# Kernel optimization log

Measured on AMD Instinct MI355X. Metric: run time of the kernel, lower is better.

## Reference

```python
import jax, jax.numpy as jnp
import numpy as np

D_MODEL = 2048
N_HEADS = 16
HEAD_DIM = D_MODEL // N_HEADS
LN_EPS = 1e-6  # flax.linen.LayerNorm default
NEG_INF = float('-inf')


def _layernorm_scale_only(x, scale):
    # flax LayerNorm with use_bias=False: normalize over last axis, scale only
    mean = jnp.mean(x, axis=-1, keepdims=True)
    var = jnp.var(x, axis=-1, keepdims=True)
    return (x - mean) * jax.lax.rsqrt(var + LN_EPS) * scale


def setup_inputs() -> dict:
    key = jax.random.key(0)
    ks = jax.random.split(key, 4)
    B, S = 2, 2048
    x = jax.random.normal(ks[0], (B, S, D_MODEL), dtype=jnp.float32)
    Wqkv = jax.random.normal(ks[1], (D_MODEL, 3 * D_MODEL), dtype=jnp.float32) * 0.02
    q_ln_scale = jnp.ones((D_MODEL,), dtype=jnp.float32)
    k_ln_scale = jnp.ones((D_MODEL,), dtype=jnp.float32)
    out_W = jax.random.normal(ks[2], (D_MODEL, D_MODEL), dtype=jnp.float32) * 0.02
    return {"x": x, "Wqkv": Wqkv, "q_ln_scale": q_ln_scale,
            "k_ln_scale": k_ln_scale, "out_W": out_W}


def reference(x, Wqkv, q_ln_scale, k_ln_scale, out_W):
    B, S, _ = x.shape
    qkv = jnp.einsum('bsd,de->bse', x, Wqkv)  # [B,S,3*D] (no bias)
    q, k, v = jnp.split(qkv, 3, axis=-1)
    # QK LayerNorm (attn_qk_ln=True, no bias)
    q = _layernorm_scale_only(q, q_ln_scale)
    k = _layernorm_scale_only(k, k_ln_scale)
    # split heads: [B,S,H,Dh]
    q = q.reshape(B, S, N_HEADS, HEAD_DIM)
    k = k.reshape(B, S, N_HEADS, HEAD_DIM)
    v = v.reshape(B, S, N_HEADS, HEAD_DIM)
    # scaled scores [B,H,S,S]
    scores = jnp.einsum('bshd,bthd->bhst', q / jnp.sqrt(jnp.float32(HEAD_DIM)), k)
    # causal mask: triu(ones, k=1) marks strictly-future positions -> -inf
    causal = jnp.triu(jnp.ones((S, S), dtype=bool), 1)
    scores = jnp.where(causal, NEG_INF, scores)
    # kv-cache mask: arange(S) < S - past_position - S = 0 -> all False (no-op
    # with past_position=0 and no layer_past), faithfully omitted.
    attn = jax.nn.softmax(scores, axis=-1)
    ctx = jnp.einsum('bhst,bthd->bshd', attn, v)  # [B,S,H,Dh]
    out = jnp.einsum('bsd,de->bse', ctx.reshape(B, S, D_MODEL), out_W)
    return out
```

## Files before the change

### kernel.cpp

```cpp
#include <hip/hip_runtime.h>


typedef float f32x4 __attribute__((ext_vector_type(4)));
typedef short s16x8 __attribute__((ext_vector_type(8)));
typedef short s16x4 __attribute__((ext_vector_type(4)));

static __device__ __forceinline__ unsigned short f2bf(float f) {
  unsigned u = __builtin_bit_cast(unsigned, f);
  unsigned r = u + 0x7fffu + ((u >> 16) & 1u);
  return (unsigned short)(r >> 16);
}
static __device__ __forceinline__ float bf2f(unsigned short s) {
  unsigned u = ((unsigned)s) << 16;
  return __builtin_bit_cast(float, u);
}

static __device__ __forceinline__ void gload_lds16(const unsigned short* g, unsigned short* l) {
  __builtin_amdgcn_global_load_lds((const __attribute__((address_space(1))) void*)g,
                                   (__attribute__((address_space(3))) void*)l, 16, 0, 0);
}

__global__ __launch_bounds__(256) void k_cvt4(const float4* __restrict__ in,
                                              s16x4* __restrict__ out, int n) {
  int i = blockIdx.x * 256 + threadIdx.x;
  if (i >= n) return;
  float4 v = in[i];
  s16x4 o = { (short)f2bf(v.x), (short)f2bf(v.y), (short)f2bf(v.z), (short)f2bf(v.w) };
  out[i] = o;
}

__global__ __launch_bounds__(256) void k_twT(const float* __restrict__ in,
                                             unsigned short* __restrict__ out,
                                             int K, int N) {
  __shared__ float tile[32][33];
  const int n0 = blockIdx.x * 32, k0 = blockIdx.y * 32;
  const int tx = threadIdx.x & 31, ty = threadIdx.x >> 5;
#pragma unroll
  for (int rr = 0; rr < 4; ++rr) {
    int kr = ty + rr * 8;
    tile[kr][tx] = in[(size_t)(k0 + kr) * N + n0 + tx];
  }
  __syncthreads();
#pragma unroll
  for (int rr = 0; rr < 4; ++rr) {
    int nr = ty + rr * 8;
    out[(size_t)(n0 + nr) * K + k0 + tx] = f2bf(tile[tx][nr]);
  }
}

template <int BF16OUT, int NFN, int MINW>
__global__ __launch_bounds__(256, MINW) void k_gw(const unsigned short* __restrict__ A,
                                                  const unsigned short* __restrict__ Bt,
                                                  void* __restrict__ Cout,
                                                  int N, int K, int npx) {
  __shared__ unsigned short sA[2 * 128 * 32];
  __shared__ unsigned short sB[2 * NFN * 32 * 32];
  const int t = threadIdx.x;
  const int wid = t >> 6, lane = t & 63, g = lane >> 4, l15 = lane & 15;
  const int wm = wid >> 1, wn = wid & 1;

  const int xcd = (int)blockIdx.x & 7, idx = (int)blockIdx.x >> 3;
  const int m0 = (idx / npx) * 128;
  const int n0 = (xcd * npx + idx % npx) * (NFN * 32);

  const int u = (t & 7) ^ ((t >> 3) & 7);
  const int srow = 2 * (t >> 3) + (u >> 2);
  const int sk = (u & 3) * 8;
  const unsigned short* pA = A  + (size_t)(m0 + srow) * K + sk;
  const unsigned short* pB = Bt + (size_t)(n0 + srow) * K + sk;

  auto stage = [&](int kt, int buf) {
#pragma unroll
    for (int j = 0; j < 2; ++j)
      gload_lds16(pA + (size_t)(j * 64) * K + kt * 32,
                  sA + buf * 4096 + j * 2048 + t * 8);
#pragma unroll
    for (int j = 0; j < NFN / 2; ++j)
      gload_lds16(pB + (size_t)(j * 64) * K + kt * 32,
                  sB + buf * (NFN * 1024) + j * 2048 + t * 8);
  };

  const int si = (((l15 & 1) * 4 + g) ^ ((l15 >> 1) & 7));
  const int baseA = (wm * 32 + (l15 >> 1)) * 64 + si * 8;
  const int baseB = (wn * NFN * 8 + (l15 >> 1)) * 64 + si * 8;

  f32x4 acc[4][NFN];
#pragma unroll
  for (int fm = 0; fm < 4; ++fm)
#pragma unroll
    for (int fn = 0; fn < NFN; ++fn) acc[fm][fn] = (f32x4){0.f, 0.f, 0.f, 0.f};

  const int NK = K >> 5;
  stage(0, 0); stage(1, 1);
  if constexpr (NFN == 8) asm volatile("s_waitcnt vmcnt(6)" ::: "memory");
  else                    asm volatile("s_waitcnt vmcnt(4)" ::: "memory");
  __builtin_amdgcn_sched_barrier(0);
  __builtin_amdgcn_s_barrier();

  for (int s = 0; s < NK; ++s) {
    const unsigned short* aT = sA + (s & 1) * 4096;
    const unsigned short* bT = sB + (s & 1) * (NFN * 1024);

    s16x8 af[4];
#pragma unroll
    for (int fm = 0; fm < 4; ++fm) af[fm] = *(const s16x8*)&aT[baseA + fm * 512];
    __builtin_amdgcn_s_setprio(1);
#pragma unroll
    for (int fn = 0; fn < NFN; ++fn) {
      s16x8 bf = *(const s16x8*)&bT[baseB + fn * 512];
#pragma unroll
      for (int fm = 0; fm < 4; ++fm)
        acc[fm][fn] = __builtin_amdgcn_mfma_f32_16x16x32_bf16(af[fm], bf, acc[fm][fn], 0, 0, 0);
    }
    __builtin_amdgcn_s_setprio(0);

    __builtin_amdgcn_sched_barrier(0);
    __builtin_amdgcn_s_barrier();
    if (s + 2 < NK) {
      stage(s + 2, s & 1);
      if constexpr (NFN == 8) asm volatile("s_waitcnt vmcnt(6)" ::: "memory");
      else                    asm volatile("s_waitcnt vmcnt(4)" ::: "memory");
    } else if (s + 1 < NK) {
      asm volatile("s_waitcnt vmcnt(0)" ::: "memory");
    }
    __builtin_amdgcn_sched_barrier(0);
    __builtin_amdgcn_s_barrier();
  }

#pragma unroll
  for (int fm = 0; fm < 4; ++fm)
#pragma unroll
    for (int fn = 0; fn < NFN; ++fn)
#pragma unroll
      for (int r = 0; r < 4; ++r) {
        const int row = m0 + wm * 64 + fm * 16 + g * 4 + r;
        const int col = n0 + wn * (NFN * 16) + fn * 16 + l15;
        if (BF16OUT)
          ((unsigned short*)Cout)[(size_t)row * N + col] = f2bf(acc[fm][fn][r]);
        else
          ((float*)Cout)[(size_t)row * N + col] = acc[fm][fn][r];
      }
}

__global__ __launch_bounds__(256) void k_ln(unsigned short* __restrict__ qkv,
                                            const float* __restrict__ qsc,
                                            const float* __restrict__ ksc) {
  __shared__ float red[8];
  const int t = threadIdx.x;
  const int w = t >> 6;
  unsigned short* base = qkv + (size_t)blockIdx.x * 6144;
#pragma unroll
  for (int part = 0; part < 2; ++part) {
    unsigned short* p = base + part * 2048 + t * 8;
    s16x8 v = *(const s16x8*)p;
    float f[8], s = 0.f, q = 0.f;
#pragma unroll
    for (int j = 0; j < 8; j++) { f[j] = bf2f((unsigned short)v[j]); s += f[j]; q += f[j] * f[j]; }
#pragma unroll
    for (int m = 1; m < 64; m <<= 1) { s += __shfl_xor(s, m); q += __shfl_xor(q, m); }
    __syncthreads();
    if ((t & 63) == 0) { red[w] = s; red[4 + w] = q; }
    __syncthreads();
    s = red[0] + red[1] + red[2] + red[3];
    q = red[4] + red[5] + red[6] + red[7];
    float mean = s * (1.f / 2048.f);
    float var = q * (1.f / 2048.f) - mean * mean;
    float inv = rsqrtf(var + 1e-6f);
    const float* sc = part ? ksc : qsc;
    float extra = part ? 1.0f : 0.12751743f;
    s16x8 o;
#pragma unroll
    for (int j = 0; j < 8; j++) o[j] = (short)f2bf((f[j] - mean) * inv * (sc[t * 8 + j] * extra));
    *(s16x8*)p = o;
  }
}

__global__ __launch_bounds__(256) void k_vT(const unsigned short* __restrict__ qkv,
                                            unsigned short* __restrict__ vt) {
  __shared__ unsigned short tl[64][136];
  const int bh = blockIdx.y;
  const int b = bh >> 4, h = bh & 15;
  const int s0 = blockIdx.x * 64;
  const int t = threadIdx.x;
#pragma unroll
  for (int it = 0; it < 4; ++it) {
    int flat = it * 256 + t;
    int r = flat >> 4, c = flat & 15;
    s16x8 v = *(const s16x8*)(qkv + (size_t)(b * 2048 + s0 + r) * 6144 + 4096 + h * 128 + c * 8);
    *((s16x8*)&tl[r][c * 8]) = v;
  }
  __syncthreads();
#pragma unroll
  for (int it = 0; it < 4; ++it) {
    int flat = it * 256 + t;
    int d = flat >> 3, cs = flat & 7;
    s16x8 o;
#pragma unroll
    for (int e = 0; e < 8; e++) {
      int key = (cs >> 2) * 32 + (e >> 2) * 16 + (cs & 3) * 4 + (e & 3);
      o[e] = (short)tl[key][d];
    }
    *(s16x8*)(vt + (size_t)(bh * 128 + d) * 2048 + s0 + cs * 8) = o;
  }
}

__global__ __launch_bounds__(512) void k_attn(const unsigned short* __restrict__ qkv,
                                              const unsigned short* __restrict__ vt,
                                              unsigned short* __restrict__ ctx) {
  __shared__ unsigned short sK[2][64 * 128];
  __shared__ unsigned short sV[2][128 * 64];
  const int t = threadIdx.x;
  const int w = t >> 6, lane = t & 63, g = lane >> 4, l15 = lane & 15;
  const int pair = blockIdx.x, h = blockIdx.y, b = blockIdx.z;
  const int qt0 = 15 - pair, qt1 = pair;
  const int n0 = 2 * qt0 + 2;
  const int NT = 34;
  const unsigned short* kbase = qkv + (size_t)(b * 2048) * 6144 + 2048 + h * 128;
  const unsigned short* vbase = vt + (size_t)((b * 16 + h) * 128) * 2048;

  auto issue_kv = [&](int k0, int bufi) {
#pragma unroll
    for (int it2 = 0; it2 < 2; ++it2) {
      int flat = it2 * 512 + t;
      int r = flat >> 4, c = flat & 15;
      gload_lds16(kbase + (size_t)(k0 + r) * 6144 + ((c ^ (r & 15)) * 8),
                  (unsigned short*)&sK[bufi][flat * 8]);
    }
#pragma unroll
    for (int it2 = 0; it2 < 2; ++it2) {
      int flat = it2 * 512 + t;
      int d = flat >> 3, z = flat & 7;
      gload_lds16(vbase + (size_t)d * 2048 + k0 + ((z ^ (d & 7)) * 8),
                  (unsigned short*)&sV[bufi][flat * 8]);
    }
  };

  s16x8 bq[4];
  auto load_q = [&](int q0) {
#pragma unroll
    for (int ks = 0; ks < 4; ++ks)
      bq[ks] = *(const s16x8*)(qkv + (size_t)(b * 2048 + q0 + w * 16 + l15) * 6144 +
                               h * 128 + (ks * 4 + g) * 8);
  };

  f32x4 o[8];
  float mrun, lrun;
  auto reset_state = [&]() {
#pragma unroll
    for (int nd = 0; nd < 8; ++nd) o[nd] = (f32x4){0.f, 0.f, 0.f, 0.f};
    mrun = -INFINITY; lrun = 0.f;
  };
  auto write_o = [&](int q0) {
    float ivr[4];
#pragma unroll
    for (int r = 0; r < 4; ++r) ivr[r] = 1.0f / __shfl(lrun, 4 * g + r);
#pragma unroll
    for (int nd = 0; nd < 8; ++nd) {
      const int col = h * 128 + nd * 16 + l15;
#pragma unroll
      for (int r = 0; r < 4; ++r) {
        const int row = b * 2048 + q0 + w * 16 + 4 * g + r;
        ctx[(size_t)row * 2048 + col] = f2bf(o[nd][r] * ivr[r]);
      }
    }
  };

  reset_state();
  load_q(qt0 * 128);
  issue_kv(0, 0);
  int cur = 0;

  for (int it = 0; it < NT; ++it) {
    const int seg = (it < n0) ? 0 : 1;
    const int qt = seg ? qt1 : qt0;
    const int kt = seg ? it - n0 : it;

    if (it + 1 < NT) {
      const int kn = (it + 1 < n0) ? it + 1 : it + 1 - n0;
      issue_kv(kn * 64, cur ^ 1);
      asm volatile("s_waitcnt vmcnt(4)" ::: "memory");
    } else {
      asm volatile("s_waitcnt vmcnt(0)" ::: "memory");
    }
    __builtin_amdgcn_sched_barrier(0);
    __builtin_amdgcn_s_barrier();

    if (seg == 1 && kt == 0) {
      write_o(qt0 * 128);
      reset_state();
      load_q(qt1 * 128);
    }

    const unsigned short* sKc = &sK[cur][0];
    const unsigned short* sVc = &sV[cur][0];

    f32x4 st[4];
#pragma unroll
    for (int mi = 0; mi < 4; ++mi) st[mi] = (f32x4){0.f, 0.f, 0.f, 0.f};
#pragma unroll
    for (int mi = 0; mi < 4; ++mi) {
#pragma unroll
      for (int ks = 0; ks < 4; ++ks) {
        s16x8 ak = *(const s16x8*)&sKc[(mi * 16 + l15) * 128 + (((ks * 4 + g) ^ l15) * 8)];
        st[mi] = __builtin_amdgcn_mfma_f32_16x16x32_bf16(ak, bq[ks], st[mi], 0, 0, 0);
      }
    }

    if (kt >= 2 * qt) {
      const int qglob = qt * 128 + w * 16 + l15;
#pragma unroll
      for (int mi = 0; mi < 4; ++mi)
#pragma unroll
        for (int r = 0; r < 4; ++r)
          if (kt * 64 + mi * 16 + 4 * g + r > qglob) st[mi][r] = -INFINITY;
    }

    float mt = -INFINITY;
#pragma unroll
    for (int mi = 0; mi < 4; ++mi)
#pragma unroll
      for (int r = 0; r < 4; ++r) mt = fmaxf(mt, st[mi][r]);
    mt = fmaxf(mt, __shfl_xor(mt, 16));
    mt = fmaxf(mt, __shfl_xor(mt, 32));

    if (!__all(mt <= mrun + 8.f)) {
      const float mnew = fmaxf(mrun, mt);
      const float alpha = exp2f(mrun - mnew);
      lrun *= alpha;
      float ar[4];
#pragma unroll
      for (int r = 0; r < 4; ++r) ar[r] = __shfl(alpha, 4 * g + r);
#pragma unroll
      for (int nd = 0; nd < 8; ++nd)
#pragma unroll
        for (int r = 0; r < 4; ++r) o[nd][r] *= ar[r];
      mrun = mnew;
    }

    float ls = 0.f;
#pragma unroll
    for (int mi = 0; mi < 4; ++mi)
#pragma unroll
      for (int r = 0; r < 4; ++r) {
        float pp = exp2f(st[mi][r] - mrun);
        st[mi][r] = pp;
        ls += pp;
      }
    ls += __shfl_xor(ls, 16);
    ls += __shfl_xor(ls, 32);
    lrun += ls;

    s16x8 pa01, pa23;
#pragma unroll
    for (int j = 0; j < 8; ++j) {
      pa01[j] = (short)f2bf(st[j >> 2][j & 3]);
      pa23[j] = (short)f2bf(st[2 + (j >> 2)][j & 3]);
    }

#pragma unroll
    for (int nd = 0; nd < 8; ++nd) {
      const int d = nd * 16 + l15;
      const int zs = d & 7;
      s16x8 bv0 = *(const s16x8*)&sVc[d * 64 + ((g ^ zs) * 8)];
      s16x8 bv1 = *(const s16x8*)&sVc[d * 64 + (((4 + g) ^ zs) * 8)];
      o[nd] = __builtin_amdgcn_mfma_f32_16x16x32_bf16(pa01, bv0, o[nd], 0, 0, 0);
      o[nd] = __builtin_amdgcn_mfma_f32_16x16x32_bf16(pa23, bv1, o[nd], 0, 0, 0);
    }

    __builtin_amdgcn_sched_barrier(0);
    __builtin_amdgcn_s_barrier();
    cur ^= 1;
  }
  write_o(qt1 * 128);
}

extern "C" void kernel_launch(void* const* d_in, const int* in_sizes, int n_in,
                              void* d_out, int out_size, void* d_ws, size_t ws_size,
                              hipStream_t stream) {
  (void)in_sizes; (void)n_in; (void)out_size; (void)ws_size;
  const float* x    = (const float*)d_in[0];
  const float* Wqkv = (const float*)d_in[1];
  const float* qsc  = (const float*)d_in[2];
  const float* ksc  = (const float*)d_in[3];
  const float* outW = (const float*)d_in[4];

  char* ws = (char*)d_ws;
  unsigned short* xb  = (unsigned short*)(ws);
  unsigned short* wT  = (unsigned short*)(ws + 16777216);
  unsigned short* owT = (unsigned short*)(ws + 41943040);
  unsigned short* qkv = (unsigned short*)(ws + 50331648);
  unsigned short* vt  = (unsigned short*)(ws + 100663296);
  unsigned short* ctx = xb;

  k_cvt4<<<8192, 256, 0, stream>>>((const float4*)x, (s16x4*)xb, 2097152);
  k_twT<<<dim3(192, 64), 256, 0, stream>>>(Wqkv, wT, 2048, 6144);
  k_twT<<<dim3(64, 64), 256, 0, stream>>>(outW, owT, 2048, 2048);
  k_gw<1, 8, 3><<<768, 256, 0, stream>>>(xb, wT, qkv, 6144, 2048, 3);
  k_ln<<<4096, 256, 0, stream>>>(qkv, qsc, ksc);
  k_vT<<<dim3(32, 32), 256, 0, stream>>>(qkv, vt);
  k_attn<<<dim3(8, 16, 2), 512, 0, stream>>>(qkv, vt, ctx);
  k_gw<0, 4, 2><<<512, 256, 0, stream>>>(ctx, owT, d_out, 2048, 2048, 2);
}
```

Baseline: 278.5 us.

## Merge prep kernels, fuse LN with V transpose, unpair attention q-tiles

Three preprocessing kernels (x conversion and two weight transposes) are merged into one launch, and the LayerNorm and V-transpose kernels are merged into another, which cuts launch count and gaps between kernels. The attention kernel drops its pairing of a long and a short causal q-tile per block. It now launches 512 blocks, one q-tile each, with heaviest tiles first, and sets a launch bound of 4 blocks per CU. This simplifies the per-iteration control flow and raises block count, but the load balancing from pairing is lost and a tail of short blocks is relied on to fill the machine instead.

```diff
diff --git a/kernel.cpp b/kernel.cpp
--- a/kernel.cpp
+++ b/kernel.cpp
@@ -20,21 +20,34 @@
                                    (__attribute__((address_space(3))) void*)l, 16, 0, 0);
 }
 
-__global__ __launch_bounds__(256) void k_cvt4(const float4* __restrict__ in,
-                                              s16x4* __restrict__ out, int n) {
-  int i = blockIdx.x * 256 + threadIdx.x;
-  if (i >= n) return;
-  float4 v = in[i];
-  s16x4 o = { (short)f2bf(v.x), (short)f2bf(v.y), (short)f2bf(v.z), (short)f2bf(v.w) };
-  out[i] = o;
-}
-
-__global__ __launch_bounds__(256) void k_twT(const float* __restrict__ in,
-                                             unsigned short* __restrict__ out,
-                                             int K, int N) {
+__global__ __launch_bounds__(256) void k_pre(const float4* __restrict__ x,
+                                             s16x4* __restrict__ xb,
+                                             const float* __restrict__ Wqkv,
+                                             unsigned short* __restrict__ wT,
+                                             const float* __restrict__ outW,
+                                             unsigned short* __restrict__ owT) {
   __shared__ float tile[32][33];
-  const int n0 = blockIdx.x * 32, k0 = blockIdx.y * 32;
-  const int tx = threadIdx.x & 31, ty = threadIdx.x >> 5;
+  const int bid = blockIdx.x, t = threadIdx.x;
+  if (bid < 8192) {
+    int i = bid * 256 + t;
+    float4 v = x[i];
+    s16x4 o = { (short)f2bf(v.x), (short)f2bf(v.y), (short)f2bf(v.z), (short)f2bf(v.w) };
+    xb[i] = o;
+    return;
+  }
+  const float* in;
+  unsigned short* out;
+  int K = 2048, N, n0, k0;
+  if (bid < 20480) {
+    int b2 = bid - 8192;
+    in = Wqkv; out = wT; N = 6144;
+    n0 = (b2 % 192) * 32; k0 = (b2 / 192) * 32;
+  } else {
+    int b2 = bid - 20480;
+    in = outW; out = owT; N = 2048;
+    n0 = (b2 & 63) * 32; k0 = (b2 >> 6) * 32;
+  }
+  const int tx = t & 31, ty = t >> 5;
 #pragma unroll
   for (int rr = 0; rr < 4; ++rr) {
     int kr = ty + rr * 8;
@@ -142,52 +155,54 @@
       }
 }
 
-__global__ __launch_bounds__(256) void k_ln(unsigned short* __restrict__ qkv,
-                                            const float* __restrict__ qsc,
-                                            const float* __restrict__ ksc) {
-  __shared__ float red[8];
-  const int t = threadIdx.x;
-  const int w = t >> 6;
-  unsigned short* base = qkv + (size_t)blockIdx.x * 6144;
-#pragma unroll
-  for (int part = 0; part < 2; ++part) {
-    unsigned short* p = base + part * 2048 + t * 8;
-    s16x8 v = *(const s16x8*)p;
-    float f[8], s = 0.f, q = 0.f;
-#pragma unroll
-    for (int j = 0; j < 8; j++) { f[j] = bf2f((unsigned short)v[j]); s += f[j]; q += f[j] * f[j]; }
-#pragma unroll
-    for (int m = 1; m < 64; m <<= 1) { s += __shfl_xor(s, m); q += __shfl_xor(q, m); }
-    __syncthreads();
-    if ((t & 63) == 0) { red[w] = s; red[4 + w] = q; }
-    __syncthreads();
-    s = red[0] + red[1] + red[2] + red[3];
-    q = red[4] + red[5] + red[6] + red[7];
-    float mean = s * (1.f / 2048.f);
-    float var = q * (1.f / 2048.f) - mean * mean;
-    float inv = rsqrtf(var + 1e-6f);
-    const float* sc = part ? ksc : qsc;
-    float extra = part ? 1.0f : 0.12751743f;
-    s16x8 o;
-#pragma unroll
-    for (int j = 0; j < 8; j++) o[j] = (short)f2bf((f[j] - mean) * inv * (sc[t * 8 + j] * extra));
-    *(s16x8*)p = o;
-  }
-}
-
-__global__ __launch_bounds__(256) void k_vT(const unsigned short* __restrict__ qkv,
-                                            unsigned short* __restrict__ vt) {
-  __shared__ unsigned short tl[64][136];
-  const int bh = blockIdx.y;
+__global__ __launch_bounds__(256) void k_lnvt(unsigned short* __restrict__ qkv,
+                                              const float* __restrict__ qsc,
+                                              const float* __restrict__ ksc,
+                                              unsigned short* __restrict__ vt) {
+  __shared__ union {
+    float red[8];
+    unsigned short tl[64][136];
+  } sm;
+  const int bid = blockIdx.x, t = threadIdx.x;
+  if (bid < 4096) {
+    const int w = t >> 6;
+    unsigned short* base = qkv + (size_t)bid * 6144;
+#pragma unroll
+    for (int part = 0; part < 2; ++part) {
+      unsigned short* p = base + part * 2048 + t * 8;
+      s16x8 v = *(const s16x8*)p;
+      float f[8], s = 0.f, q = 0.f;
+#pragma unroll
+      for (int j = 0; j < 8; j++) { f[j] = bf2f((unsigned short)v[j]); s += f[j]; q += f[j] * f[j]; }
+#pragma unroll
+      for (int m = 1; m < 64; m <<= 1) { s += __shfl_xor(s, m); q += __shfl_xor(q, m); }
+      __syncthreads();
+      if ((t & 63) == 0) { sm.red[w] = s; sm.red[4 + w] = q; }
+      __syncthreads();
+      s = sm.red[0] + sm.red[1] + sm.red[2] + sm.red[3];
+      q = sm.red[4] + sm.red[5] + sm.red[6] + sm.red[7];
+      float mean = s * (1.f / 2048.f);
+      float var = q * (1.f / 2048.f) - mean * mean;
+      float inv = rsqrtf(var + 1e-6f);
+      const float* sc = part ? ksc : qsc;
+      float extra = part ? 1.0f : 0.12751743f;
+      s16x8 o;
+#pragma unroll
+      for (int j = 0; j < 8; j++) o[j] = (short)f2bf((f[j] - mean) * inv * (sc[t * 8 + j] * extra));
+      *(s16x8*)p = o;
+    }
+    return;
+  }
+  const int b2 = bid - 4096;
+  const int bh = b2 >> 5;
   const int b = bh >> 4, h = bh & 15;
-  const int s0 = blockIdx.x * 64;
-  const int t = threadIdx.x;
+  const int s0 = (b2 & 31) * 64;
 #pragma unroll
   for (int it = 0; it < 4; ++it) {
     int flat = it * 256 + t;
     int r = flat >> 4, c = flat & 15;
     s16x8 v = *(const s16x8*)(qkv + (size_t)(b * 2048 + s0 + r) * 6144 + 4096 + h * 128 + c * 8);
-    *((s16x8*)&tl[r][c * 8]) = v;
+    *((s16x8*)&sm.tl[r][c * 8]) = v;
   }
   __syncthreads();
 #pragma unroll
@@ -198,23 +213,22 @@
 #pragma unroll
     for (int e = 0; e < 8; e++) {
       int key = (cs >> 2) * 32 + (e >> 2) * 16 + (cs & 3) * 4 + (e & 3);
-      o[e] = (short)tl[key][d];
+      o[e] = (short)sm.tl[key][d];
     }
     *(s16x8*)(vt + (size_t)(bh * 128 + d) * 2048 + s0 + cs * 8) = o;
   }
 }
 
-__global__ __launch_bounds__(512) void k_attn(const unsigned short* __restrict__ qkv,
-                                              const unsigned short* __restrict__ vt,
-                                              unsigned short* __restrict__ ctx) {
+__global__ __launch_bounds__(512, 4) void k_attn(const unsigned short* __restrict__ qkv,
+                                                 const unsigned short* __restrict__ vt,
+                                                 unsigned short* __restrict__ ctx) {
   __shared__ unsigned short sK[2][64 * 128];
   __shared__ unsigned short sV[2][128 * 64];
   const int t = threadIdx.x;
   const int w = t >> 6, lane = t & 63, g = lane >> 4, l15 = lane & 15;
-  const int pair = blockIdx.x, h = blockIdx.y, b = blockIdx.z;
-  const int qt0 = 15 - pair, qt1 = pair;
-  const int n0 = 2 * qt0 + 2;
-  const int NT = 34;
+  const int qt = 15 - (int)blockIdx.x, h = blockIdx.y, b = blockIdx.z;
+  const int q0 = qt * 128;
+  const int NT = 2 * qt + 2;
   const unsigned short* kbase = qkv + (size_t)(b * 2048) * 6144 + 2048 + h * 128;
   const unsigned short* vbase = vt + (size_t)((b * 16 + h) * 128) * 2048;
 
@@ -236,60 +250,28 @@
   };
 
   s16x8 bq[4];
-  auto load_q = [&](int q0) {
-#pragma unroll
-    for (int ks = 0; ks < 4; ++ks)
-      bq[ks] = *(const s16x8*)(qkv + (size_t)(b * 2048 + q0 + w * 16 + l15) * 6144 +
-                               h * 128 + (ks * 4 + g) * 8);
-  };
+#pragma unroll
+  for (int ks = 0; ks < 4; ++ks)
+    bq[ks] = *(const s16x8*)(qkv + (size_t)(b * 2048 + q0 + w * 16 + l15) * 6144 +
+                             h * 128 + (ks * 4 + g) * 8);
 
   f32x4 o[8];
-  float mrun, lrun;
-  auto reset_state = [&]() {
-#pragma unroll
-    for (int nd = 0; nd < 8; ++nd) o[nd] = (f32x4){0.f, 0.f, 0.f, 0.f};
-    mrun = -INFINITY; lrun = 0.f;
-  };
-  auto write_o = [&](int q0) {
-    float ivr[4];
-#pragma unroll
-    for (int r = 0; r < 4; ++r) ivr[r] = 1.0f / __shfl(lrun, 4 * g + r);
-#pragma unroll
-    for (int nd = 0; nd < 8; ++nd) {
-      const int col = h * 128 + nd * 16 + l15;
-#pragma unroll
-      for (int r = 0; r < 4; ++r) {
-        const int row = b * 2048 + q0 + w * 16 + 4 * g + r;
-        ctx[(size_t)row * 2048 + col] = f2bf(o[nd][r] * ivr[r]);
-      }
-    }
-  };
-
-  reset_state();
-  load_q(qt0 * 128);
+#pragma unroll
+  for (int nd = 0; nd < 8; ++nd) o[nd] = (f32x4){0.f, 0.f, 0.f, 0.f};
+  float mrun = -INFINITY, lrun = 0.f;
+
   issue_kv(0, 0);
   int cur = 0;
 
-  for (int it = 0; it < NT; ++it) {
-    const int seg = (it < n0) ? 0 : 1;
-    const int qt = seg ? qt1 : qt0;
-    const int kt = seg ? it - n0 : it;
-
-    if (it + 1 < NT) {
-      const int kn = (it + 1 < n0) ? it + 1 : it + 1 - n0;
-      issue_kv(kn * 64, cur ^ 1);
+  for (int kt = 0; kt < NT; ++kt) {
+    if (kt + 1 < NT) {
+      issue_kv((kt + 1) * 64, cur ^ 1);
       asm volatile("s_waitcnt vmcnt(4)" ::: "memory");
     } else {
       asm volatile("s_waitcnt vmcnt(0)" ::: "memory");
     }
     __builtin_amdgcn_sched_barrier(0);
     __builtin_amdgcn_s_barrier();
-
-    if (seg == 1 && kt == 0) {
-      write_o(qt0 * 128);
-      reset_state();
-      load_q(qt1 * 128);
-    }
 
     const unsigned short* sKc = &sK[cur][0];
     const unsigned short* sVc = &sV[cur][0];
@@ -307,7 +289,7 @@
     }
 
     if (kt >= 2 * qt) {
-      const int qglob = qt * 128 + w * 16 + l15;
+      const int qglob = q0 + w * 16 + l15;
 #pragma unroll
       for (int mi = 0; mi < 4; ++mi)
 #pragma unroll
@@ -371,7 +353,19 @@
     __builtin_amdgcn_s_barrier();
     cur ^= 1;
   }
-  write_o(qt1 * 128);
+
+  float ivr[4];
+#pragma unroll
+  for (int r = 0; r < 4; ++r) ivr[r] = 1.0f / __shfl(lrun, 4 * g + r);
+#pragma unroll
+  for (int nd = 0; nd < 8; ++nd) {
+    const int col = h * 128 + nd * 16 + l15;
+#pragma unroll
+    for (int r = 0; r < 4; ++r) {
+      const int row = b * 2048 + q0 + w * 16 + 4 * g + r;
+      ctx[(size_t)row * 2048 + col] = f2bf(o[nd][r] * ivr[r]);
+    }
+  }
 }
 
 extern "C" void kernel_launch(void* const* d_in, const int* in_sizes, int n_in,
@@ -392,12 +386,9 @@
   unsigned short* vt  = (unsigned short*)(ws + 100663296);
   unsigned short* ctx = xb;
 
-  k_cvt4<<<8192, 256, 0, stream>>>((const float4*)x, (s16x4*)xb, 2097152);
-  k_twT<<<dim3(192, 64), 256, 0, stream>>>(Wqkv, wT, 2048, 6144);
-  k_twT<<<dim3(64, 64), 256, 0, stream>>>(outW, owT, 2048, 2048);
+  k_pre<<<24576, 256, 0, stream>>>((const float4*)x, (s16x4*)xb, Wqkv, wT, outW, owT);
   k_gw<1, 8, 3><<<768, 256, 0, stream>>>(xb, wT, qkv, 6144, 2048, 3);
-  k_ln<<<4096, 256, 0, stream>>>(qkv, qsc, ksc);
-  k_vT<<<dim3(32, 32), 256, 0, stream>>>(qkv, vt);
-  k_attn<<<dim3(8, 16, 2), 512, 0, stream>>>(qkv, vt, ctx);
+  k_lnvt<<<5120, 256, 0, stream>>>(qkv, qsc, ksc, vt);
+  k_attn<<<dim3(16, 16, 2), 512, 0, stream>>>(qkv, vt, ctx);
   k_gw<0, 4, 2><<<512, 256, 0, stream>>>(ctx, owT, d_out, 2048, 2048, 2);
 }
```

Result: slower. 287.2 us (+3.2%).
